# Kernel optimization log

Measured on AMD Instinct MI355X. Metric: run time of the kernel, lower is better.

The kernel has to match this reference:

```python
import jax, jax.numpy as jnp
import numpy as np

PAD_ID = 0    # scibert [PAD]
SEP_ID = 103  # scibert [SEP]
IGNORE = 100


def setup_inputs() -> dict:
    key = jax.random.key(0)
    ks = jax.random.split(key, 8)
    B, S, D, T = 64, 512, 768, 2
    return {
        "sequence_output": jax.random.normal(ks[0], (B, S, D), dtype=jnp.float32),
        "input_ids": jax.random.randint(ks[1], (B, S), 0, 31090, dtype=jnp.int64),
        "labels": jax.random.randint(ks[2], (B, S), 0, 2, dtype=jnp.int64),
        "W": jax.random.normal(ks[3], (T, D), dtype=jnp.float32) * 0.02,
        "b": jax.random.normal(ks[4], (T,), dtype=jnp.float32) * 0.02,
        "start_trans": jax.random.normal(ks[5], (T,), dtype=jnp.float32) * 0.1,
        "end_trans": jax.random.normal(ks[6], (T,), dtype=jnp.float32) * 0.1,
        "trans": jax.random.normal(ks[7], (T, T), dtype=jnp.float32) * 0.1,
    }


def _crf_llh_token_mean(em, tags, start, end, trans):
    # em: [B,S,T], tags: [B,S]; mask=None in torchcrf => all-ones mask.
    B, S, T = em.shape
    # numerator: score of the gold path
    em_tag = jnp.take_along_axis(em, tags[..., None], axis=2)[..., 0]        # [B,S]
    tr_tag = trans[tags[:, :-1], tags[:, 1:]]                                 # [B,S-1]
    score = start[tags[:, 0]] + em_tag.sum(1) + tr_tag.sum(1) + end[tags[:, -1]]
    # denominator: forward algorithm over time (scan over S-1 tiny steps)
    alpha0 = start[None, :] + em[:, 0]                                        # [B,T]
    em_rest = jnp.swapaxes(em[:, 1:], 0, 1)                                   # [S-1,B,T]

    def step(alpha, em_t):
        # alpha[b,i] + trans[i,j] + em_t[b,j] -> logsumexp over i
        nxt = jax.nn.logsumexp(alpha[:, :, None] + trans[None], axis=1) + em_t
        return nxt, None

    alpha, _ = jax.lax.scan(step, alpha0, em_rest)
    logZ = jax.nn.logsumexp(alpha + end[None, :], axis=1)                     # [B]
    llh = score - logZ
    # reduction='token_mean' with all-ones mask -> sum / (B*S)
    return llh.sum() / jnp.float32(B * S)


def _crf_viterbi(em, start, end, trans):
    # em: [B,S,T] -> decoded tags [B,S] int32
    B, S, T = em.shape
    score0 = start[None, :] + em[:, 0]                                        # [B,T]
    em_rest = jnp.swapaxes(em[:, 1:], 0, 1)                                   # [S-1,B,T]

    def vstep(score, em_t):
        cand = score[:, :, None] + trans[None] + em_t[:, None, :]             # [B,T,T]
        return cand.max(axis=1), cand.argmax(axis=1).astype(jnp.int32)

    final, hist = jax.lax.scan(vstep, score0, em_rest)                        # hist [S-1,B,T]
    final = final + end[None, :]
    last = jnp.argmax(final, axis=1).astype(jnp.int32)                        # [B]

    def back(tag, bp_t):
        prev = jnp.take_along_axis(bp_t, tag[:, None], axis=1)[:, 0]
        return prev, prev

    _, prevs = jax.lax.scan(back, last, hist, reverse=True)                   # [S-1,B]
    tags = jnp.concatenate([prevs, last[None, :]], axis=0)                    # [S,B]
    return jnp.swapaxes(tags, 0, 1)                                           # [B,S]


def reference(sequence_output, input_ids, labels, W, b, start_trans, end_trans, trans):
    mask = (input_ids != PAD_ID) & (input_ids != SEP_ID) & (labels != IGNORE)  # [B,S] bool
    seq = sequence_output * mask[..., None].astype(sequence_output.dtype)
    labels_m = labels * mask.astype(labels.dtype)
    # probablities = relu(hidden2tag(seq))
    em = jax.nn.relu(jnp.einsum("bsd,td->bst", seq, W) + b)                    # [B,S,2]
    loss = _crf_llh_token_mean(em, labels_m, start_trans, end_trans, trans)
    target_emissions = _crf_viterbi(em, start_trans, end_trans, trans).astype(jnp.float32)
    return (loss, target_emissions, labels_m, mask)
```

## Files before the change

### kernel.cpp

```cpp
#include <hip/hip_runtime.h>

#define BB 64
#define SS 512
#define DD 768
#define NROWS (BB*SS)
#define NEG (-1e30f)
#define NCH 16
#define CL  32

__global__ __launch_bounds__(256) void k_emissions(
    const float* __restrict__ seq,
    const int*   __restrict__ input_ids,
    const int*   __restrict__ labels,
    const float* __restrict__ W,
    const float* __restrict__ bias,
    float* __restrict__ em_t,
    int*   __restrict__ tags_t,
    float* __restrict__ out)
{
    const int lane = threadIdx.x & 63;
    const int wid  = blockIdx.x * 4 + (threadIdx.x >> 6);
    const int base = wid * 4;

    const float4* W4 = (const float4*)W;
    float4 w0[3], w1[3];
#pragma unroll
    for (int j = 0; j < 3; ++j) {
        w0[j] = W4[j*64 + lane];
        w1[j] = W4[192 + j*64 + lane];
    }
    const float b0 = bias[0], b1 = bias[1];

    const float4* s4 = (const float4*)seq;
    float4 v[4][3];
#pragma unroll
    for (int r = 0; r < 4; ++r)
#pragma unroll
        for (int j = 0; j < 3; ++j)
            v[r][j] = s4[(size_t)(base + r)*192 + j*64 + lane];

    float d0[4], d1[4];
#pragma unroll
    for (int r = 0; r < 4; ++r) {
        float a0 = 0.f, a1 = 0.f;
#pragma unroll
        for (int j = 0; j < 3; ++j) {
            float4 x = v[r][j];
            a0 += x.x*w0[j].x + x.y*w0[j].y + x.z*w0[j].z + x.w*w0[j].w;
            a1 += x.x*w1[j].x + x.y*w1[j].y + x.z*w1[j].z + x.w*w1[j].w;
        }
        d0[r] = a0; d1[r] = a1;
    }
#pragma unroll
    for (int m = 32; m >= 1; m >>= 1) {
#pragma unroll
        for (int r = 0; r < 4; ++r) {
            d0[r] += __shfl_xor(d0[r], m, 64);
            d1[r] += __shfl_xor(d1[r], m, 64);
        }
    }
    if (lane == 0) {
        const int4 idv = *(const int4*)(input_ids + base);
        const int4 lbv = *(const int4*)(labels + base);
        const int ida[4] = {idv.x, idv.y, idv.z, idv.w};
        const int lba[4] = {lbv.x, lbv.y, lbv.z, lbv.w};
#pragma unroll
        for (int r = 0; r < 4; ++r) {
            const int row = base + r;
            const int id = ida[r], lab = lba[r];
            const int msk = (id != 0 && id != 103 && lab != 100) ? 1 : 0;
            const int lm  = lab * msk;
            const float e0 = fmaxf((msk ? d0[r] : 0.f) + b0, 0.f);
            const float e1 = fmaxf((msk ? d1[r] : 0.f) + b1, 0.f);
            const int b_ = row >> 9, s_ = row & 511;
            *(float2*)(em_t + (s_*BB + b_)*2) = make_float2(e0, e1);
            tags_t[s_*BB + b_] = lm;
            out[1 + NROWS   + row] = (float)lm;
            out[1 + 2*NROWS + row] = (float)msk;
        }
    }
}

__device__ __forceinline__ float lse2(float x, float y) {
    float m = fmaxf(x, y);
    float d = fminf(x, y) - m;
    return m + __logf(1.f + __expf(d));
}

#define STEP_L(e_, g_) do { \
    float n0 = lse2(P00 + t00, P01 + t10) + (e_).x; \
    float n1 = lse2(P00 + t01, P01 + t11) + (e_).y; \
    float n2 = lse2(P10 + t00, P11 + t10) + (e_).x; \
    float n3 = lse2(P10 + t01, P11 + t11) + (e_).y; \
    P00 = n0; P01 = n1; P10 = n2; P11 = n3; \
    score += (ptag ? ((g_) ? t11 : t10) : ((g_) ? t01 : t00)) \
           + ((g_) ? (e_).y : (e_).x); \
    ptag = (g_); \
} while (0)

#define STEP_VP(e_) do { \
    float n0 = fmaxf(V00 + t00, V01 + t10) + (e_).x; \
    float n1 = fmaxf(V00 + t01, V01 + t11) + (e_).y; \
    float n2 = fmaxf(V10 + t00, V11 + t10) + (e_).x; \
    float n3 = fmaxf(V10 + t01, V11 + t11) + (e_).y; \
    V00 = n0; V01 = n1; V10 = n2; V11 = n3; \
} while (0)

#define STEP_BP(k_, e_) do { \
    float c00 = v0 + t00, c10 = v1 + t10; \
    float c01 = v0 + t01, c11 = v1 + t11; \
    int bp0 = (c10 > c00); int bp1 = (c11 > c01); \
    v0 = fmaxf(c00, c10) + (e_).x; v1 = fmaxf(c01, c11) + (e_).y; \
    acc |= (unsigned)(bp0 | (bp1 << 1)) << (2 * ((k_) & 15)); \
    if ((((k_) & 15)) == 15) { bp_sh[b*33 + ((k_) >> 4)] = acc; acc = 0u; } \
} while (0)

__global__ __launch_bounds__(1024) void k_crf(
    const float* __restrict__ em_t,
    const int*   __restrict__ tags_t,
    const float* __restrict__ start,
    const float* __restrict__ endt,
    const float* __restrict__ trans,
    float* __restrict__ out)
{
    __shared__ float4 logP4[NCH][BB];
    __shared__ float  scoreP[NCH][BB];
    __shared__ float4 vitP4[NCH][BB];
    __shared__ float2 vbound[NCH][BB];
    __shared__ unsigned int bp_sh[BB*33];
    __shared__ unsigned int tagbits[BB*17];

    const int tid = threadIdx.x;
    const int b   = tid & 63;
    const int c   = tid >> 6;
    const int k0  = c * CL;
    const float t00 = trans[0], t01 = trans[1], t10 = trans[2], t11 = trans[3];
    const float s0 = start[0], s1 = start[1];
    const float en0 = endt[0], en1 = endt[1];
    const float2* em2 = (const float2*)em_t;

    if (blockIdx.x == 0) {
        float2 e[8]; int g[8];
        float P00, P01, P10, P11, score; int ptag;
#pragma unroll
        for (int i = 0; i < 8; ++i) {
            e[i] = em2[(k0+i)*BB + b];
            g[i] = tags_t[(k0+i)*BB + b];
        }
        if (c == 0) {
            P00 = 0.f; P01 = NEG; P10 = NEG; P11 = 0.f;
            score = g[0] ? (s1 + e[0].y) : (s0 + e[0].x);
        } else {
            int pt = tags_t[(k0-1)*BB + b];
            P00 = t00 + e[0].x; P01 = t01 + e[0].y;
            P10 = t10 + e[0].x; P11 = t11 + e[0].y;
            score = (pt ? (g[0] ? t11 : t10) : (g[0] ? t01 : t00))
                  + (g[0] ? e[0].y : e[0].x);
        }
        ptag = g[0];
#pragma unroll
        for (int i = 1; i < 8; ++i) STEP_L(e[i], g[i]);
#pragma unroll
        for (int j = 1; j < 4; ++j) {
#pragma unroll
            for (int i = 0; i < 8; ++i) {
                e[i] = em2[(k0 + j*8 + i)*BB + b];
                g[i] = tags_t[(k0 + j*8 + i)*BB + b];
            }
#pragma unroll
            for (int i = 0; i < 8; ++i) STEP_L(e[i], g[i]);
        }
        logP4[c][b] = make_float4(P00, P01, P10, P11);
        scoreP[c][b] = score;
        __syncthreads();
        if (c == 0) {
            float2 em0v = em2[b];
            float a0 = s0 + em0v.x, a1 = s1 + em0v.y, sc = 0.f;
#pragma unroll
            for (int cc = 0; cc < NCH; ++cc) {
                float4 P = logP4[cc][b];
                float n0 = lse2(a0 + P.x, a1 + P.z);
                float n1 = lse2(a0 + P.y, a1 + P.w);
                a0 = n0; a1 = n1;
                sc += scoreP[cc][b];
            }
            int tagL = tags_t[511*BB + b];
            sc += tagL ? en1 : en0;
            float logZ = lse2(a0 + en0, a1 + en1);
            float llh = sc - logZ;
#pragma unroll
            for (int m = 32; m >= 1; m >>= 1) llh += __shfl_xor(llh, m, 64);
            if (b == 0) out[0] = llh / (float)NROWS;
        }
    } else {
        float2 e[8];
        float V00, V01, V10, V11;
#pragma unroll
        for (int i = 0; i < 8; ++i) e[i] = em2[(k0+i)*BB + b];
        if (c == 0) {
            V00 = 0.f; V01 = NEG; V10 = NEG; V11 = 0.f;
        } else {
            V00 = t00 + e[0].x; V01 = t01 + e[0].y;
            V10 = t10 + e[0].x; V11 = t11 + e[0].y;
        }
#pragma unroll
        for (int i = 1; i < 8; ++i) STEP_VP(e[i]);
#pragma unroll
        for (int j = 1; j < 4; ++j) {
#pragma unroll
            for (int i = 0; i < 8; ++i) e[i] = em2[(k0 + j*8 + i)*BB + b];
#pragma unroll
            for (int i = 0; i < 8; ++i) STEP_VP(e[i]);
        }
        vitP4[c][b] = make_float4(V00, V01, V10, V11);
        __syncthreads();

        int last = 0;
        if (c == 0) {
            float2 em0v = em2[b];
            float v0 = s0 + em0v.x, v1 = s1 + em0v.y;
            vbound[0][b] = make_float2(v0, v1);
#pragma unroll
            for (int cc = 0; cc < NCH; ++cc) {
                float4 V = vitP4[cc][b];
                float n0 = fmaxf(v0 + V.x, v1 + V.z);
                float n1 = fmaxf(v0 + V.y, v1 + V.w);
                v0 = n0; v1 = n1;
                if (cc < NCH-1) vbound[cc+1][b] = make_float2(v0, v1);
            }
            last = (v1 + en1 > v0 + en0) ? 1 : 0;
        }
        __syncthreads();

        {
            float2 vb = vbound[c][b];
            float v0 = vb.x, v1 = vb.y;
            unsigned acc = 0u;
#pragma unroll
            for (int i = 0; i < 8; ++i) e[i] = em2[(k0+i)*BB + b];
            if (c != 0) STEP_BP(k0, e[0]);
#pragma unroll
            for (int i = 1; i < 8; ++i) STEP_BP(k0 + i, e[i]);
#pragma unroll
            for (int j = 1; j < 4; ++j) {
#pragma unroll
                for (int i = 0; i < 8; ++i) e[i] = em2[(k0 + j*8 + i)*BB + b];
#pragma unroll
                for (int i = 0; i < 8; ++i) STEP_BP(k0 + j*8 + i, e[i]);
            }
        }
        __syncthreads();

        if (c == 0) {
            int tag = last;
            unsigned acc = ((unsigned)tag) << 31;
            for (int w = 31; w >= 0; --w) {
                unsigned word = bp_sh[b*33 + w];
                const int kbase = w * 16;
#pragma unroll
                for (int i = 15; i >= 0; --i) {
                    if (kbase + i == 0) continue;
                    int prev = (word >> (2*i + tag)) & 1;
                    int pos = kbase + i - 1;
                    acc |= (unsigned)prev << (pos & 31);
                    if ((pos & 31) == 0) { tagbits[b*17 + (pos >> 5)] = acc; acc = 0u; }
                    tag = prev;
                }
            }
        }
        __syncthreads();

        for (int idx = tid; idx < NROWS; idx += 1024) {
            const int bq = idx >> 9, k = idx & 511;
            unsigned wd = tagbits[bq*17 + (k >> 5)];
            out[1 + idx] = (float)((wd >> (k & 31)) & 1);
        }
    }
}

extern "C" void kernel_launch(void* const* d_in, const int* in_sizes, int n_in,
                              void* d_out, int out_size, void* d_ws, size_t ws_size,
                              hipStream_t stream) {
    const float* seq    = (const float*)d_in[0];
    const int*   ids    = (const int*)  d_in[1];
    const int*   labels = (const int*)  d_in[2];
    const float* W      = (const float*)d_in[3];
    const float* bias   = (const float*)d_in[4];
    const float* start  = (const float*)d_in[5];
    const float* endt   = (const float*)d_in[6];
    const float* trans  = (const float*)d_in[7];
    float* out = (float*)d_out;

    float* em_t   = (float*)d_ws;
    int*   tags_t = (int*)((char*)d_ws + (size_t)65536*sizeof(float));

    k_emissions<<<2048, 256, 0, stream>>>(seq, ids, labels, W, bias, em_t, tags_t, out);
    k_crf<<<2, 1024, 0, stream>>>(em_t, tags_t, start, endt, trans, out);
}
```

Baseline: 180.3 us.

## Use exp-domain forward recursion and parallel chunked Viterbi backtrace

Result: faster. 173.6 us (-3.7%).

```diff
diff --git a/kernel.cpp b/kernel.cpp
--- a/kernel.cpp
+++ b/kernel.cpp
@@ -87,15 +87,24 @@
     return m + __logf(1.f + __expf(d));
 }
 
-#define STEP_L(e_, g_) do { \
-    float n0 = lse2(P00 + t00, P01 + t10) + (e_).x; \
-    float n1 = lse2(P00 + t01, P01 + t11) + (e_).y; \
-    float n2 = lse2(P10 + t00, P11 + t10) + (e_).x; \
-    float n3 = lse2(P10 + t01, P11 + t11) + (e_).y; \
-    P00 = n0; P01 = n1; P10 = n2; P11 = n3; \
+#define STEP_LE(e_, g_) do { \
+    float Ex = __expf((e_).x), Ey = __expf((e_).y); \
+    float B00 = X00*Ex, B10 = X10*Ex, B01 = X01*Ey, B11 = X11*Ey; \
+    float n00 = fmaf(p00, B00, p01*B10); \
+    float n01 = fmaf(p00, B01, p01*B11); \
+    float n10 = fmaf(p10, B00, p11*B10); \
+    float n11 = fmaf(p10, B01, p11*B11); \
+    p00 = n00; p01 = n01; p10 = n10; p11 = n11; \
     score += (ptag ? ((g_) ? t11 : t10) : ((g_) ? t01 : t00)) \
            + ((g_) ? (e_).y : (e_).x); \
     ptag = (g_); \
+} while (0)
+
+#define RENORM() do { \
+    float m0 = fmaxf(p00, p01), m1 = fmaxf(p10, p11); \
+    float r0 = __builtin_amdgcn_rcpf(m0), r1 = __builtin_amdgcn_rcpf(m1); \
+    p00 *= r0; p01 *= r0; p10 *= r1; p11 *= r1; \
+    lc0 += __logf(m0); lc1 += __logf(m1); \
 } while (0)
 
 #define STEP_VP(e_) do { \
@@ -106,13 +115,15 @@
     V00 = n0; V01 = n1; V10 = n2; V11 = n3; \
 } while (0)
 
-#define STEP_BP(k_, e_) do { \
+#define STEP_BPF(i_, e_) do { \
     float c00 = v0 + t00, c10 = v1 + t10; \
     float c01 = v0 + t01, c11 = v1 + t11; \
     int bp0 = (c10 > c00); int bp1 = (c11 > c01); \
     v0 = fmaxf(c00, c10) + (e_).x; v1 = fmaxf(c01, c11) + (e_).y; \
-    acc |= (unsigned)(bp0 | (bp1 << 1)) << (2 * ((k_) & 15)); \
-    if ((((k_) & 15)) == 15) { bp_sh[b*33 + ((k_) >> 4)] = acc; acc = 0u; } \
+    unsigned two = (unsigned)(bp0 | (bp1 << 1)); \
+    if ((i_) < 16) w0 |= two << (2*(i_)); else w1 |= two << (2*((i_)-16)); \
+    int nF0 = bp0 ? F1 : F0; int nF1 = bp1 ? F1 : F0; \
+    F0 = nF0; F1 = nF1; \
 } while (0)
 
 __global__ __launch_bounds__(1024) void k_crf(
@@ -127,7 +138,8 @@
     __shared__ float  scoreP[NCH][BB];
     __shared__ float4 vitP4[NCH][BB];
     __shared__ float2 vbound[NCH][BB];
-    __shared__ unsigned int bp_sh[BB*33];
+    __shared__ unsigned char Fsh[NCH][BB];
+    __shared__ int lastSh[BB];
     __shared__ unsigned int tagbits[BB*17];
 
     const int tid = threadIdx.x;
@@ -140,26 +152,30 @@
     const float2* em2 = (const float2*)em_t;
 
     if (blockIdx.x == 0) {
+        const float X00 = __expf(t00), X01 = __expf(t01),
+                    X10 = __expf(t10), X11 = __expf(t11);
         float2 e[8]; int g[8];
-        float P00, P01, P10, P11, score; int ptag;
+        float p00, p01, p10, p11, lc0 = 0.f, lc1 = 0.f, score;
+        int ptag;
 #pragma unroll
         for (int i = 0; i < 8; ++i) {
             e[i] = em2[(k0+i)*BB + b];
             g[i] = tags_t[(k0+i)*BB + b];
         }
         if (c == 0) {
-            P00 = 0.f; P01 = NEG; P10 = NEG; P11 = 0.f;
+            p00 = 1.f; p01 = 0.f; p10 = 0.f; p11 = 1.f;
             score = g[0] ? (s1 + e[0].y) : (s0 + e[0].x);
         } else {
             int pt = tags_t[(k0-1)*BB + b];
-            P00 = t00 + e[0].x; P01 = t01 + e[0].y;
-            P10 = t10 + e[0].x; P11 = t11 + e[0].y;
+            float Ex = __expf(e[0].x), Ey = __expf(e[0].y);
+            p00 = X00*Ex; p01 = X01*Ey; p10 = X10*Ex; p11 = X11*Ey;
             score = (pt ? (g[0] ? t11 : t10) : (g[0] ? t01 : t00))
                   + (g[0] ? e[0].y : e[0].x);
         }
         ptag = g[0];
 #pragma unroll
-        for (int i = 1; i < 8; ++i) STEP_L(e[i], g[i]);
+        for (int i = 1; i < 8; ++i) STEP_LE(e[i], g[i]);
+        RENORM();
 #pragma unroll
         for (int j = 1; j < 4; ++j) {
 #pragma unroll
@@ -168,9 +184,14 @@
                 g[i] = tags_t[(k0 + j*8 + i)*BB + b];
             }
 #pragma unroll
-            for (int i = 0; i < 8; ++i) STEP_L(e[i], g[i]);
-        }
-        logP4[c][b] = make_float4(P00, P01, P10, P11);
+            for (int i = 0; i < 8; ++i) STEP_LE(e[i], g[i]);
+            RENORM();
+        }
+        float P00L = fmaxf(__logf(p00) + lc0, NEG);
+        float P01L = fmaxf(__logf(p01) + lc0, NEG);
+        float P10L = fmaxf(__logf(p10) + lc1, NEG);
+        float P11L = fmaxf(__logf(p11) + lc1, NEG);
+        logP4[c][b] = make_float4(P00L, P01L, P10L, P11L);
         scoreP[c][b] = score;
         __syncthreads();
         if (c == 0) {
@@ -193,10 +214,10 @@
             if (b == 0) out[0] = llh / (float)NROWS;
         }
     } else {
-        float2 e[8];
+        float2 e[32];
+#pragma unroll
+        for (int i = 0; i < 32; ++i) e[i] = em2[(k0+i)*BB + b];
         float V00, V01, V10, V11;
-#pragma unroll
-        for (int i = 0; i < 8; ++i) e[i] = em2[(k0+i)*BB + b];
         if (c == 0) {
             V00 = 0.f; V01 = NEG; V10 = NEG; V11 = 0.f;
         } else {
@@ -204,18 +225,10 @@
             V10 = t10 + e[0].x; V11 = t11 + e[0].y;
         }
 #pragma unroll
-        for (int i = 1; i < 8; ++i) STEP_VP(e[i]);
-#pragma unroll
-        for (int j = 1; j < 4; ++j) {
-#pragma unroll
-            for (int i = 0; i < 8; ++i) e[i] = em2[(k0 + j*8 + i)*BB + b];
-#pragma unroll
-            for (int i = 0; i < 8; ++i) STEP_VP(e[i]);
-        }
+        for (int i = 1; i < 32; ++i) STEP_VP(e[i]);
         vitP4[c][b] = make_float4(V00, V01, V10, V11);
         __syncthreads();
 
-        int last = 0;
         if (c == 0) {
             float2 em0v = em2[b];
             float v0 = s0 + em0v.x, v1 = s1 + em0v.y;
@@ -228,45 +241,35 @@
                 v0 = n0; v1 = n1;
                 if (cc < NCH-1) vbound[cc+1][b] = make_float2(v0, v1);
             }
-            last = (v1 + en1 > v0 + en0) ? 1 : 0;
-        }
-        __syncthreads();
-
+            lastSh[b] = (v1 + en1 > v0 + en0) ? 1 : 0;
+        }
+        __syncthreads();
+
+        unsigned w0 = 0u, w1 = 0u;
+        int F0 = 0, F1 = 1;
         {
             float2 vb = vbound[c][b];
             float v0 = vb.x, v1 = vb.y;
-            unsigned acc = 0u;
-#pragma unroll
-            for (int i = 0; i < 8; ++i) e[i] = em2[(k0+i)*BB + b];
-            if (c != 0) STEP_BP(k0, e[0]);
-#pragma unroll
-            for (int i = 1; i < 8; ++i) STEP_BP(k0 + i, e[i]);
-#pragma unroll
-            for (int j = 1; j < 4; ++j) {
-#pragma unroll
-                for (int i = 0; i < 8; ++i) e[i] = em2[(k0 + j*8 + i)*BB + b];
-#pragma unroll
-                for (int i = 0; i < 8; ++i) STEP_BP(k0 + j*8 + i, e[i]);
+            if (c != 0) STEP_BPF(0, e[0]);
+#pragma unroll
+            for (int i = 1; i < 32; ++i) STEP_BPF(i, e[i]);
+        }
+        Fsh[c][b] = (unsigned char)(F0 | (F1 << 1));
+        __syncthreads();
+
+        {
+            int t = lastSh[b];
+            for (int cc = NCH-1; cc > c; --cc)
+                t = (Fsh[cc][b] >> t) & 1;
+            unsigned word = ((unsigned)t) << 31;
+#pragma unroll
+            for (int i = 31; i >= 1; --i) {
+                unsigned pair = ((i >= 16) ? (w1 >> (2*(i-16)))
+                                           : (w0 >> (2*i))) & 3u;
+                t = (int)((pair >> t) & 1u);
+                word |= ((unsigned)t) << (i - 1);
             }
-        }
-        __syncthreads();
-
-        if (c == 0) {
-            int tag = last;
-            unsigned acc = ((unsigned)tag) << 31;
-            for (int w = 31; w >= 0; --w) {
-                unsigned word = bp_sh[b*33 + w];
-                const int kbase = w * 16;
-#pragma unroll
-                for (int i = 15; i >= 0; --i) {
-                    if (kbase + i == 0) continue;
-                    int prev = (word >> (2*i + tag)) & 1;
-                    int pos = kbase + i - 1;
-                    acc |= (unsigned)prev << (pos & 31);
-                    if ((pos & 31) == 0) { tagbits[b*17 + (pos >> 5)] = acc; acc = 0u; }
-                    tag = prev;
-                }
-            }
+            tagbits[b*17 + c] = word;
         }
         __syncthreads();
 
```
